# Performance work log

Hardware: AMD Instinct MI355X
Metric: run time of the kernel (lower is better)

## Reference

```python
import jax, jax.numpy as jnp
import numpy as np
from jax import lax

HIDDEN = 64
EPS = 1e-6


def setup_inputs() -> dict:
    key = jax.random.key(0)
    ks = jax.random.split(key, 7)
    B, S, H = 2048, 2048, HIDDEN
    scale_ih = 1.0 / np.sqrt(2.0)
    scale_hh = 1.0 / np.sqrt(H)
    return {
        "residuals": jax.random.normal(ks[0], (B, S), dtype=jnp.float32),
        "W_ih_w": jax.random.uniform(ks[1], (H, 2), jnp.float32, -scale_ih, scale_ih),
        "W_ih_b": jax.random.uniform(ks[2], (H,), jnp.float32, -scale_ih, scale_ih),
        "W_hh_w": jax.random.uniform(ks[3], (H, H), jnp.float32, -scale_hh, scale_hh),
        "W_hh_b": jax.random.uniform(ks[4], (H,), jnp.float32, -scale_hh, scale_hh),
        "fc_w": jax.random.uniform(ks[5], (1, H), jnp.float32, -scale_hh, scale_hh),
        "fc_b": jax.random.uniform(ks[6], (1,), jnp.float32, -scale_hh, scale_hh),
    }


def reference(residuals, W_ih_w, W_ih_b, W_hh_w, W_hh_b, fc_w, fc_b):
    B, S = residuals.shape
    H = W_hh_w.shape[0]
    # torch.var is unbiased (ddof=1)
    sigma0 = jnp.var(residuals, axis=1, ddof=1)  # (B,)
    h0 = jnp.zeros((B, H), dtype=residuals.dtype)

    def step(carry, eps_prev):
        h, sigma = carry  # (B,H), (B,)
        inp = jnp.stack([eps_prev * eps_prev, sigma], axis=1)  # (B,2)
        h = inp @ W_ih_w.T + W_ih_b + h @ W_hh_w.T + W_hh_b  # (B,H)
        sigma = jax.nn.softplus(h @ fc_w.T + fc_b)[:, 0] + EPS  # (B,)
        return (h, sigma), sigma

    # eps at steps t=1..S-1 uses residuals[:, t-1]
    (_, _), sigmas = lax.scan(step, (h0, sigma0), residuals[:, :-1].T)  # (S-1, B)
    cond_vars = jnp.concatenate([sigma0[:, None], sigmas.T], axis=1)  # (B, S)
    return cond_vars
```

## Files before the change

### kernel.cpp

```cpp
#include <hip/hip_runtime.h>

#define S_LEN 2048

typedef float f32x4 __attribute__((ext_vector_type(4)));

__device__ __forceinline__ float rlane(float v, int l) {
    return __int_as_float(__builtin_amdgcn_readlane(__float_as_int(v), l));
}

template<int CTRL, int RM>
__device__ __forceinline__ float dpp_add(float v) {
    int t = __builtin_amdgcn_update_dpp(0, __float_as_int(v), CTRL, RM, 0xF, true);
    return v + __int_as_float(t);
}
__device__ __forceinline__ float wave_sum(float v) {
    v = dpp_add<0x111, 0xF>(v);
    v = dpp_add<0x112, 0xF>(v);
    v = dpp_add<0x114, 0xF>(v);
    v = dpp_add<0x118, 0xF>(v);
    v = dpp_add<0x142, 0xA>(v);
    v = dpp_add<0x143, 0xC>(v);
    return rlane(v, 63);
}
__device__ __forceinline__ float half_sum(float v, bool hf) {
    v = dpp_add<0x111, 0xF>(v);
    v = dpp_add<0x112, 0xF>(v);
    v = dpp_add<0x114, 0xF>(v);
    v = dpp_add<0x118, 0xF>(v);
    v = dpp_add<0x142, 0xA>(v);
    const float lo = rlane(v, 31);
    const float hi = rlane(v, 63);
    return hf ? hi : lo;
}

#if __has_builtin(__builtin_amdgcn_exp2f)
#define EXP2F(x) __builtin_amdgcn_exp2f(x)
#else
#define EXP2F(x) exp2f(x)
#endif
#if __has_builtin(__builtin_amdgcn_logf)
#define LOG2F(x) __builtin_amdgcn_logf(x)
#else
#define LOG2F(x) __log2f(x)
#endif

__global__ __launch_bounds__(64) void garch_setup(
    const float* __restrict__ Wih, const float* __restrict__ bih,
    const float* __restrict__ Whh, const float* __restrict__ bhh,
    const float* __restrict__ fcw, const float* __restrict__ fcb,
    float* __restrict__ ws)
{
    const int lane = threadIdx.x;
    __shared__ __align__(16) float ub[64];
    __shared__ float alpS[32], betS[32];

    float wr[64];
#pragma unroll
    for (int k = 0; k < 64; ++k) wr[k] = Whh[k * 64 + lane];

    const float w0l = Wih[lane * 2], w1l = Wih[lane * 2 + 1];
    const float bl = bih[lane] + bhh[lane];
    const float fl = fcw[lane];
    const float Kc = 1.44269504088896340736f;

    const float A0  = Kc * wave_sum(fl * w0l);
    const float b0t = wave_sum(fl * w1l);
    const float C   = Kc * (wave_sum(fl * bl) + fcb[0]);
    if (lane == 0) { alpS[0] = A0; betS[0] = b0t; }
    float gpre = C, ginf = C;

    ub[lane] = fl;
    asm volatile("" ::: "memory");
    const f32x4* uq4 = (const f32x4*)ub;
    float u;
    {
        float n0 = 0.f, n1 = 0.f, n2 = 0.f, n3 = 0.f;
#pragma unroll
        for (int q = 0; q < 16; ++q) {
            const f32x4 uq = uq4[q];
            n0 = fmaf(wr[4 * q + 0], uq.x, n0);
            n1 = fmaf(wr[4 * q + 1], uq.y, n1);
            n2 = fmaf(wr[4 * q + 2], uq.z, n2);
            n3 = fmaf(wr[4 * q + 3], uq.w, n3);
        }
        u = (n0 + n1) + (n2 + n3);
    }
#pragma unroll 1
    for (int i = 1; i < 48; ++i) {
        const float daK = Kc * wave_sum(u * w0l);
        const float dbT = wave_sum(u * w1l);
        const float dgK = Kc * wave_sum(u * bl);
        if (lane == 0 && i < 32) { alpS[i] = daK; betS[i] = dbT; }
        gpre += (lane >= i) ? dgK : 0.f;
        ginf += dgK;
        ub[lane] = u;
        asm volatile("" ::: "memory");
        float n0 = 0.f, n1 = 0.f, n2 = 0.f, n3 = 0.f;
#pragma unroll
        for (int q = 0; q < 16; ++q) {
            const f32x4 uq = uq4[q];
            n0 = fmaf(wr[4 * q + 0], uq.x, n0);
            n1 = fmaf(wr[4 * q + 1], uq.y, n1);
            n2 = fmaf(wr[4 * q + 2], uq.z, n2);
            n3 = fmaf(wr[4 * q + 3], uq.w, n3);
        }
        u = (n0 + n1) + (n2 + n3);
    }
    asm volatile("" ::: "memory");

    for (int f = lane; f < 1024; f += 64) {
        const int l = f >> 5, j = f & 31;
        const int m = (l - j) & 31;
        ws[f]        = (m < 4) ? 0.f : alpS[m];
        ws[1024 + f] = (m < 4) ? 0.f : betS[m];
    }
    if (lane < 32) ws[2048 + lane] = gpre;
    if (lane == 0) ws[2080] = ginf;
    if (lane < 4) { ws[2081 + lane] = betS[lane]; ws[2085 + lane] = alpS[lane]; }
}

__attribute__((amdgpu_flat_work_group_size(512, 512)))
__attribute__((amdgpu_waves_per_eu(4, 8)))
__global__ void garch_main(
    const float* __restrict__ res, const float* __restrict__ ws,
    float* __restrict__ out)
{
    __shared__ __align__(16) float ring[1024];

    const int tid  = threadIdx.x;
    const int lane = tid & 63;
    const int wv   = tid >> 6;
    const int l    = lane & 31;
    const bool hf  = (lane >= 32);

    float* __restrict__ ringw = &ring[wv * 128 + (hf ? 64 : 0)];

    const f32x4* wst = (const f32x4*)ws;
    f32x4 ca[8], cb[8];
#pragma unroll
    for (int q = 0; q < 8; ++q) { ca[q] = wst[l * 8 + q]; cb[q] = wst[256 + l * 8 + q]; }
    asm("" : "+v"(ca[0]), "+v"(ca[1]), "+v"(ca[2]), "+v"(ca[3]),
             "+v"(ca[4]), "+v"(ca[5]), "+v"(ca[6]), "+v"(ca[7]),
             "+v"(cb[0]), "+v"(cb[1]), "+v"(cb[2]), "+v"(cb[3]),
             "+v"(cb[4]), "+v"(cb[5]), "+v"(cb[6]), "+v"(cb[7]));

    const float ginf = ws[2080];
    const float b0 = ws[2081], b1 = ws[2082], b2 = ws[2083], b3 = ws[2084];
    const float Ka0 = ws[2085], Ka1 = ws[2086], Ka2 = ws[2087], Ka3 = ws[2088];
    const float Kc  = 1.44269504088896340736f;
    const float LN2 = 0.69314718055994530942f;

    const int gw = blockIdx.x * 8 + wv;
    const int rp = gw >> 2;
    const int p  = gw & 3;
    const float* __restrict__ row  = res + (size_t)(2 * rp + (hf ? 1 : 0)) * S_LEN;
    float* __restrict__       orow = out + (size_t)(2 * rp + (hf ? 1 : 0)) * S_LEN;

    const int rotaddr = ((lane & 32) | ((l + 31) & 31)) << 2;

#define FIR4(DST, SB) { \
    const int a0_ = ((SB) << 5) + l; \
    const float x0_ = ringw[a0_]; \
    const float x1_ = ringw[(a0_ - 1) & 63]; \
    const float x2_ = ringw[(a0_ - 2) & 63]; \
    const float x3_ = ringw[(a0_ - 3) & 63]; \
    (DST) = fmaf(Ka3, x3_, fmaf(Ka2, x2_, fmaf(Ka1, x1_, Ka0 * x0_))); }

#define BCASTI(DST, V, IDX) { \
    const float lo_ = rlane((V), (IDX)); \
    const float hi_ = rlane((V), 32 + (IDX)); \
    (DST) = hf ? hi_ : lo_; }

    float acc, sigK, carry, p1, p2, p3, ldn, varh = 0.f;
    float vout = 0.f;
    int c0w, warm;

    if (p == 0) {
        float s1 = 0.f, s2 = 0.f;
#pragma unroll 8
        for (int i = 0; i < 64; ++i) {
            const float x = row[i * 32 + l];
            s1 += x;
            s2 = fmaf(x, x, s2);
        }
        s1 = half_sum(s1, hf);
        s2 = half_sum(s2, hf);
        const float mean = s1 * (1.0f / S_LEN);
        varh = (s2 - s1 * mean) * (1.0f / (S_LEN - 1));
        sigK = Kc * varh;
        carry = sigK;

        const float e0 = row[l], e1 = row[32 + l];
        ringw[l] = e0 * e0;
        ringw[32 + l] = 0.f;
        asm volatile("" ::: "memory");
        float e4C;
        FIR4(e4C, 0);
        acc = ws[2048 + l] + e4C;
        BCASTI(p1, acc, 0); BCASTI(p2, acc, 1); BCASTI(p3, acc, 2);
        ringw[32 + l] = e1 * e1;
        asm volatile("" ::: "memory");
        ldn = row[64 + l];
        c0w = 0; warm = 0;
    } else {
        const int cw0 = p * 16 - 2;
        const float eP = row[(cw0 - 1) * 32 + l];
        const float eC = row[cw0 * 32 + l];
        const float eN = row[(cw0 + 1) * 32 + l];
        ringw[((cw0 - 1) & 1) * 32 + l] = eP * eP;
        ringw[(cw0 & 1) * 32 + l]       = eC * eC;
        asm volatile("" ::: "memory");
        float e4C;
        FIR4(e4C, cw0 & 1);
        acc = ginf + e4C;
        const f32x4* pq = (const f32x4*)(ringw + ((cw0 - 1) & 1) * 32);
#pragma unroll
        for (int q = 0; q < 8; ++q) {
            const f32x4 eq = pq[q];
#pragma unroll
            for (int w = 0; w < 4; ++w) {
                const int j = 4 * q + w;
                const float cf = (j > l) ? ca[q][w] : 0.f;
                acc = fmaf(cf, eq[w], acc);
            }
        }
        BCASTI(p1, acc, 0); BCASTI(p2, acc, 1); BCASTI(p3, acc, 2);
        sigK = 0.f; carry = 0.f;
        ringw[((cw0 + 1) & 1) * 32 + l] = eN * eN;
        asm volatile("" ::: "memory");
        ldn = row[(cw0 + 2) * 32 + l];
        c0w = cw0; warm = 2;
    }

    const int ncc = 16 + warm;
    const bool p0 = (p == 0);

#pragma unroll 1
    for (int cc = 0; cc < ncc; ++cc) {
        const int c = c0w + cc;
        const int s = c & 1;
        float e4N;
        FIR4(e4N, s ^ 1);
        const float sigchunk = carry;

        const f32x4* ringq = (const f32x4*)(ringw + (s << 5));
        f32x4 curA = ringq[0], curB = ringq[1];
        f32x4 nxtA, nxtB;

#pragma unroll
        for (int jg = 0; jg < 4; ++jg) {
            if (jg < 3) { nxtA = ringq[(jg + 1) * 2]; nxtB = ringq[(jg + 1) * 2 + 1]; }
#pragma unroll
            for (int k = 0; k < 8; ++k) {
                const int jj = jg * 8 + k;
                const float ash = ca[jj >> 2][jj & 3];
                const float bsh = cb[jj >> 2][jj & 3];
                const float e2j = (k < 4) ? curA[k] : curB[k - 4];
                const float xp = fmaf(b0, sigK, p1);
                acc = fmaf(bsh, sigK, acc);
                acc = fmaf(ash, e2j, acc);
                const bool mine = (l == jj);
                acc = mine ? ginf : acc;
                const float tlo = rlane(acc, (jj + 3) & 31);
                const float thi = rlane(acc, 32 + ((jj + 3) & 31));
                float t = hf ? thi : tlo;
                if (jj >= 29) {
                    const float clo = rlane(e4N, jj - 29);
                    const float chi = rlane(e4N, 32 + (jj - 29));
                    t += hf ? chi : clo;
                }
                p1 = fmaf(b1, sigK, p2);
                p2 = fmaf(b2, sigK, p3);
                p3 = fmaf(b3, sigK, t);
                const float ee = EXP2F(-__builtin_fabsf(xp));
                sigK = fmaxf(xp, 0.f) + LOG2F(1.0f + ee);
                vout = mine ? sigK : vout;
            }
            if (jg < 3) { curA = nxtA; curB = nxtB; }
        }

        if (cc >= warm) {
            const float rotv = __int_as_float(
                __builtin_amdgcn_ds_bpermute(rotaddr, __float_as_int(vout)));
            const float sv = (l == 0) ? sigchunk : rotv;
            float outv = fmaf(sv, LN2, 1e-6f);
            if (p0 && cc == 0) outv = (l == 0) ? varh : outv;
            orow[(c << 5) + l] = outv;
        }
        {
            const float c1v = rlane(vout, 31);
            const float c2v = rlane(vout, 63);
            carry = hf ? c2v : c1v;
        }
        acc += e4N;
        ringw[(s << 5) + l] = ldn * ldn;
        const int nc3 = (c + 3 < 63) ? (c + 3) : 63;
        ldn = row[nc3 * 32 + l];
        asm volatile("" ::: "memory");
    }
#undef FIR4
#undef BCASTI
}

extern "C" void kernel_launch(void* const* d_in, const int* in_sizes, int n_in,
                              void* d_out, int out_size, void* d_ws, size_t ws_size,
                              hipStream_t stream) {
    const float* res = (const float*)d_in[0];
    const float* Wih = (const float*)d_in[1];
    const float* bih = (const float*)d_in[2];
    const float* Whh = (const float*)d_in[3];
    const float* bhh = (const float*)d_in[4];
    const float* fcw = (const float*)d_in[5];
    const float* fcb = (const float*)d_in[6];
    float* out = (float*)d_out;
    float* ws  = (float*)d_ws;

    hipLaunchKernelGGL(garch_setup, dim3(1), dim3(64), 0, stream,
                       Wih, bih, Whh, bhh, fcw, fcb, ws);
    hipLaunchKernelGGL(garch_main, dim3(512), dim3(512), 0, stream,
                       res, ws, out);
}
```

Before: 190.6 us.

## Fuse setup into main kernel and split each row pair across eight waves

Removes the separate single-wave setup launch. Each block now recomputes the GARCH coefficient tables in wave 0 from a shared-memory copy of W_hh and keeps them in LDS rather than registers. Work per row pair is split into eight shorter segments of 8 chunks (previously four of 16), with 1024 blocks instead of 512, which shortens the serial critical path. The cost is redundant setup in every block (47 serial matvec iterations before a barrier), extra LDS reads of the coefficients inside the inner loop, and proportionally more warm-up overhead per segment.

```diff
diff --git a/kernel.cpp b/kernel.cpp
--- a/kernel.cpp
+++ b/kernel.cpp
@@ -44,88 +44,24 @@
 #define LOG2F(x) __log2f(x)
 #endif
 
-__global__ __launch_bounds__(64) void garch_setup(
-    const float* __restrict__ Wih, const float* __restrict__ bih,
-    const float* __restrict__ Whh, const float* __restrict__ bhh,
-    const float* __restrict__ fcw, const float* __restrict__ fcb,
-    float* __restrict__ ws)
-{
-    const int lane = threadIdx.x;
-    __shared__ __align__(16) float ub[64];
-    __shared__ float alpS[32], betS[32];
-
-    float wr[64];
-#pragma unroll
-    for (int k = 0; k < 64; ++k) wr[k] = Whh[k * 64 + lane];
-
-    const float w0l = Wih[lane * 2], w1l = Wih[lane * 2 + 1];
-    const float bl = bih[lane] + bhh[lane];
-    const float fl = fcw[lane];
-    const float Kc = 1.44269504088896340736f;
-
-    const float A0  = Kc * wave_sum(fl * w0l);
-    const float b0t = wave_sum(fl * w1l);
-    const float C   = Kc * (wave_sum(fl * bl) + fcb[0]);
-    if (lane == 0) { alpS[0] = A0; betS[0] = b0t; }
-    float gpre = C, ginf = C;
-
-    ub[lane] = fl;
-    asm volatile("" ::: "memory");
-    const f32x4* uq4 = (const f32x4*)ub;
-    float u;
-    {
-        float n0 = 0.f, n1 = 0.f, n2 = 0.f, n3 = 0.f;
-#pragma unroll
-        for (int q = 0; q < 16; ++q) {
-            const f32x4 uq = uq4[q];
-            n0 = fmaf(wr[4 * q + 0], uq.x, n0);
-            n1 = fmaf(wr[4 * q + 1], uq.y, n1);
-            n2 = fmaf(wr[4 * q + 2], uq.z, n2);
-            n3 = fmaf(wr[4 * q + 3], uq.w, n3);
-        }
-        u = (n0 + n1) + (n2 + n3);
-    }
-#pragma unroll 1
-    for (int i = 1; i < 48; ++i) {
-        const float daK = Kc * wave_sum(u * w0l);
-        const float dbT = wave_sum(u * w1l);
-        const float dgK = Kc * wave_sum(u * bl);
-        if (lane == 0 && i < 32) { alpS[i] = daK; betS[i] = dbT; }
-        gpre += (lane >= i) ? dgK : 0.f;
-        ginf += dgK;
-        ub[lane] = u;
-        asm volatile("" ::: "memory");
-        float n0 = 0.f, n1 = 0.f, n2 = 0.f, n3 = 0.f;
-#pragma unroll
-        for (int q = 0; q < 16; ++q) {
-            const f32x4 uq = uq4[q];
-            n0 = fmaf(wr[4 * q + 0], uq.x, n0);
-            n1 = fmaf(wr[4 * q + 1], uq.y, n1);
-            n2 = fmaf(wr[4 * q + 2], uq.z, n2);
-            n3 = fmaf(wr[4 * q + 3], uq.w, n3);
-        }
-        u = (n0 + n1) + (n2 + n3);
-    }
-    asm volatile("" ::: "memory");
-
-    for (int f = lane; f < 1024; f += 64) {
-        const int l = f >> 5, j = f & 31;
-        const int m = (l - j) & 31;
-        ws[f]        = (m < 4) ? 0.f : alpS[m];
-        ws[1024 + f] = (m < 4) ? 0.f : betS[m];
-    }
-    if (lane < 32) ws[2048 + lane] = gpre;
-    if (lane == 0) ws[2080] = ginf;
-    if (lane < 4) { ws[2081 + lane] = betS[lane]; ws[2085 + lane] = alpS[lane]; }
-}
-
 __attribute__((amdgpu_flat_work_group_size(512, 512)))
-__attribute__((amdgpu_waves_per_eu(4, 8)))
-__global__ void garch_main(
-    const float* __restrict__ res, const float* __restrict__ ws,
+__attribute__((amdgpu_waves_per_eu(8)))
+__global__ void garch_fused(
+    const float* __restrict__ res,
+    const float* __restrict__ Wih,
+    const float* __restrict__ bih,
+    const float* __restrict__ Whh,
+    const float* __restrict__ bhh,
+    const float* __restrict__ fcw,
+    const float* __restrict__ fcb,
     float* __restrict__ out)
 {
+    __shared__ __align__(16) float Wl[4096];
+    __shared__ __align__(16) float tabA[1024];
+    __shared__ __align__(16) float tabB[1024];
     __shared__ __align__(16) float ring[1024];
+    __shared__ __align__(16) float ubuf[64];
+    __shared__ float alpS[32], betS[32], gpreS[32], scS[4];
 
     const int tid  = threadIdx.x;
     const int lane = tid & 63;
@@ -133,29 +69,87 @@
     const int l    = lane & 31;
     const bool hf  = (lane >= 32);
 
-    float* __restrict__ ringw = &ring[wv * 128 + (hf ? 64 : 0)];
-
-    const f32x4* wst = (const f32x4*)ws;
-    f32x4 ca[8], cb[8];
-#pragma unroll
-    for (int q = 0; q < 8; ++q) { ca[q] = wst[l * 8 + q]; cb[q] = wst[256 + l * 8 + q]; }
-    asm("" : "+v"(ca[0]), "+v"(ca[1]), "+v"(ca[2]), "+v"(ca[3]),
-             "+v"(ca[4]), "+v"(ca[5]), "+v"(ca[6]), "+v"(ca[7]),
-             "+v"(cb[0]), "+v"(cb[1]), "+v"(cb[2]), "+v"(cb[3]),
-             "+v"(cb[4]), "+v"(cb[5]), "+v"(cb[6]), "+v"(cb[7]));
-
-    const float ginf = ws[2080];
-    const float b0 = ws[2081], b1 = ws[2082], b2 = ws[2083], b3 = ws[2084];
-    const float Ka0 = ws[2085], Ka1 = ws[2086], Ka2 = ws[2087], Ka3 = ws[2088];
     const float Kc  = 1.44269504088896340736f;
     const float LN2 = 0.69314718055994530942f;
 
-    const int gw = blockIdx.x * 8 + wv;
-    const int rp = gw >> 2;
-    const int p  = gw & 3;
+    {
+        const f32x4* w4 = (const f32x4*)Whh;
+        f32x4* wl4 = (f32x4*)Wl;
+        for (int i = tid; i < 1024; i += 512) wl4[i] = w4[i];
+    }
+    __syncthreads();
+
+    if (wv == 0) {
+        const float w0l = Wih[lane * 2], w1l = Wih[lane * 2 + 1];
+        const float blp = bih[lane] + bhh[lane];
+        const float fl  = fcw[lane];
+
+        const float A0  = Kc * wave_sum(fl * w0l);
+        const float b0t = wave_sum(fl * w1l);
+        const float Cg  = Kc * (wave_sum(fl * blp) + fcb[0]);
+        if (lane == 0) { alpS[0] = A0; betS[0] = b0t; }
+        float gpre_ = Cg, ginf_ = Cg;
+
+        ubuf[lane] = fl;
+        asm volatile("" ::: "memory");
+        const f32x4* uq4 = (const f32x4*)ubuf;
+        float u;
+        {
+            float n0 = 0.f, n1 = 0.f, n2 = 0.f, n3 = 0.f;
+#pragma unroll 4
+            for (int q = 0; q < 16; ++q) {
+                const f32x4 uq = uq4[q];
+                n0 = fmaf(Wl[(4 * q + 0) * 64 + lane], uq.x, n0);
+                n1 = fmaf(Wl[(4 * q + 1) * 64 + lane], uq.y, n1);
+                n2 = fmaf(Wl[(4 * q + 2) * 64 + lane], uq.z, n2);
+                n3 = fmaf(Wl[(4 * q + 3) * 64 + lane], uq.w, n3);
+            }
+            u = (n0 + n1) + (n2 + n3);
+        }
+#pragma unroll 1
+        for (int i = 1; i < 48; ++i) {
+            const float daK = Kc * wave_sum(u * w0l);
+            const float dbT = wave_sum(u * w1l);
+            const float dgK = Kc * wave_sum(u * blp);
+            if (lane == 0 && i < 32) { alpS[i] = daK; betS[i] = dbT; }
+            gpre_ += (lane >= i) ? dgK : 0.f;
+            ginf_ += dgK;
+            ubuf[lane] = u;
+            asm volatile("" ::: "memory");
+            float n0 = 0.f, n1 = 0.f, n2 = 0.f, n3 = 0.f;
+#pragma unroll 4
+            for (int q = 0; q < 16; ++q) {
+                const f32x4 uq = uq4[q];
+                n0 = fmaf(Wl[(4 * q + 0) * 64 + lane], uq.x, n0);
+                n1 = fmaf(Wl[(4 * q + 1) * 64 + lane], uq.y, n1);
+                n2 = fmaf(Wl[(4 * q + 2) * 64 + lane], uq.z, n2);
+                n3 = fmaf(Wl[(4 * q + 3) * 64 + lane], uq.w, n3);
+            }
+            u = (n0 + n1) + (n2 + n3);
+        }
+        asm volatile("" ::: "memory");
+        for (int f = lane; f < 1024; f += 64) {
+            const int lr = f >> 5, jc = f & 31;
+            const int m = (lr - jc) & 31;
+            const int dst = (((jc >> 2) * 32 + lr) << 2) + (jc & 3);
+            tabA[dst] = (m < 4) ? 0.f : alpS[m];
+            tabB[dst] = (m < 4) ? 0.f : betS[m];
+        }
+        if (lane < 32) gpreS[lane] = gpre_;
+        if (lane == 0) scS[0] = ginf_;
+    }
+    __syncthreads();
+
+    const float ginf = scS[0];
+    const float bb0 = betS[0], bb1 = betS[1], bb2 = betS[2], bb3 = betS[3];
+    const float Ka0 = alpS[0], Ka1 = alpS[1], Ka2 = alpS[2], Ka3 = alpS[3];
+
+    const int rp = blockIdx.x;
+    const int p  = wv;
     const float* __restrict__ row  = res + (size_t)(2 * rp + (hf ? 1 : 0)) * S_LEN;
     float* __restrict__       orow = out + (size_t)(2 * rp + (hf ? 1 : 0)) * S_LEN;
 
+    float* __restrict__ ringw = &ring[wv * 128 + (hf ? 64 : 0)];
     const int rotaddr = ((lane & 32) | ((l + 31) & 31)) << 2;
 
 #define FIR4(DST, SB) { \
@@ -171,6 +165,9 @@
     const float hi_ = rlane((V), 32 + (IDX)); \
     (DST) = hf ? hi_ : lo_; }
 
+    const f32x4* tA4 = (const f32x4*)tabA;
+    const f32x4* tB4 = (const f32x4*)tabB;
+
     float acc, sigK, carry, p1, p2, p3, ldn, varh = 0.f;
     float vout = 0.f;
     int c0w, warm;
@@ -196,14 +193,14 @@
         asm volatile("" ::: "memory");
         float e4C;
         FIR4(e4C, 0);
-        acc = ws[2048 + l] + e4C;
+        acc = gpreS[l] + e4C;
         BCASTI(p1, acc, 0); BCASTI(p2, acc, 1); BCASTI(p3, acc, 2);
         ringw[32 + l] = e1 * e1;
         asm volatile("" ::: "memory");
         ldn = row[64 + l];
         c0w = 0; warm = 0;
     } else {
-        const int cw0 = p * 16 - 2;
+        const int cw0 = 8 * p - 1;
         const float eP = row[(cw0 - 1) * 32 + l];
         const float eC = row[cw0 * 32 + l];
         const float eN = row[(cw0 + 1) * 32 + l];
@@ -216,11 +213,12 @@
         const f32x4* pq = (const f32x4*)(ringw + ((cw0 - 1) & 1) * 32);
 #pragma unroll
         for (int q = 0; q < 8; ++q) {
+            const f32x4 aqv = tA4[q * 32 + l];
             const f32x4 eq = pq[q];
 #pragma unroll
             for (int w = 0; w < 4; ++w) {
                 const int j = 4 * q + w;
-                const float cf = (j > l) ? ca[q][w] : 0.f;
+                const float cf = (j > l) ? aqv[w] : 0.f;
                 acc = fmaf(cf, eq[w], acc);
             }
         }
@@ -229,10 +227,10 @@
         ringw[((cw0 + 1) & 1) * 32 + l] = eN * eN;
         asm volatile("" ::: "memory");
         ldn = row[(cw0 + 2) * 32 + l];
-        c0w = cw0; warm = 2;
+        c0w = cw0; warm = 1;
     }
 
-    const int ncc = 16 + warm;
+    const int ncc = 8 + warm;
     const bool p0 = (p == 0);
 
 #pragma unroll 1
@@ -241,42 +239,39 @@
         const int s = c & 1;
         float e4N;
         FIR4(e4N, s ^ 1);
+        const float ginfE = ginf + e4N;
         const float sigchunk = carry;
-
         const f32x4* ringq = (const f32x4*)(ringw + (s << 5));
-        f32x4 curA = ringq[0], curB = ringq[1];
-        f32x4 nxtA, nxtB;
 
 #pragma unroll
         for (int jg = 0; jg < 4; ++jg) {
-            if (jg < 3) { nxtA = ringq[(jg + 1) * 2]; nxtB = ringq[(jg + 1) * 2 + 1]; }
+            const f32x4 caq0 = tA4[(2 * jg) * 32 + l];
+            const f32x4 caq1 = tA4[(2 * jg + 1) * 32 + l];
+            const f32x4 cbq0 = tB4[(2 * jg) * 32 + l];
+            const f32x4 cbq1 = tB4[(2 * jg + 1) * 32 + l];
+            const f32x4 curA = ringq[jg * 2];
+            const f32x4 curB = ringq[jg * 2 + 1];
 #pragma unroll
             for (int k = 0; k < 8; ++k) {
-                const int jj = jg * 8 + k;
-                const float ash = ca[jj >> 2][jj & 3];
-                const float bsh = cb[jj >> 2][jj & 3];
+                const int jj = (jg << 3) + k;
+                const float ash = (k < 4) ? caq0[k] : caq1[k - 4];
+                const float bsh = (k < 4) ? cbq0[k] : cbq1[k - 4];
                 const float e2j = (k < 4) ? curA[k] : curB[k - 4];
-                const float xp = fmaf(b0, sigK, p1);
+                const float xp = fmaf(bb0, sigK, p1);
                 acc = fmaf(bsh, sigK, acc);
                 acc = fmaf(ash, e2j, acc);
                 const bool mine = (l == jj);
-                acc = mine ? ginf : acc;
+                acc = mine ? ginfE : acc;
                 const float tlo = rlane(acc, (jj + 3) & 31);
                 const float thi = rlane(acc, 32 + ((jj + 3) & 31));
-                float t = hf ? thi : tlo;
-                if (jj >= 29) {
-                    const float clo = rlane(e4N, jj - 29);
-                    const float chi = rlane(e4N, 32 + (jj - 29));
-                    t += hf ? chi : clo;
-                }
-                p1 = fmaf(b1, sigK, p2);
-                p2 = fmaf(b2, sigK, p3);
-                p3 = fmaf(b3, sigK, t);
+                const float t = hf ? thi : tlo;
+                p1 = fmaf(bb1, sigK, p2);
+                p2 = fmaf(bb2, sigK, p3);
+                p3 = fmaf(bb3, sigK, t);
                 const float ee = EXP2F(-__builtin_fabsf(xp));
                 sigK = fmaxf(xp, 0.f) + LOG2F(1.0f + ee);
                 vout = mine ? sigK : vout;
             }
-            if (jg < 3) { curA = nxtA; curB = nxtB; }
         }
 
         if (cc >= warm) {
@@ -292,7 +287,6 @@
             const float c2v = rlane(vout, 63);
             carry = hf ? c2v : c1v;
         }
-        acc += e4N;
         ringw[(s << 5) + l] = ldn * ldn;
         const int nc3 = (c + 3 < 63) ? (c + 3) : 63;
         ldn = row[nc3 * 32 + l];
@@ -313,10 +307,7 @@
     const float* fcw = (const float*)d_in[5];
     const float* fcb = (const float*)d_in[6];
     float* out = (float*)d_out;
-    float* ws  = (float*)d_ws;
-
-    hipLaunchKernelGGL(garch_setup, dim3(1), dim3(64), 0, stream,
-                       Wih, bih, Whh, bhh, fcw, fcb, ws);
-    hipLaunchKernelGGL(garch_main, dim3(512), dim3(512), 0, stream,
-                       res, ws, out);
-}
+
+    hipLaunchKernelGGL(garch_fused, dim3(1024), dim3(512), 0, stream,
+                       res, Wih, bih, Whh, bhh, fcw, fcb, out);
+}
```

New measurement: 189.0 us. About the same (-0.8%).
